# Performance work log

Measured on AMD Instinct MI355X. Metric: run time of the kernel, lower is better.

Reference implementation:

```python
import jax, jax.numpy as jnp
import numpy as np

S = 128          # hidden mul for 0e and 1o in the GVP
M_OUT = 256      # 2*n_dets*el_emb_dim = 2*8*16
N_DETS = 8
FACTOR = 2 * N_DETS  # mul_to_axis factor = 16
EPS = 1e-8


def _gvp_layer(s, v, Wh, Wu, Wm, bm, activate):
    # s: (..., S) scalars (0e); v: (..., S, 3) vectors (1o)
    Vh = jnp.einsum('...mt,mh->...ht', v, Wh)                 # hidden vectors
    vn = jnp.sqrt(jnp.sum(Vh * Vh, axis=-1) + EPS)            # invariant norms
    sm = jnp.concatenate([s, vn], axis=-1) @ Wm + bm          # scalar channel
    Vu = jnp.einsum('...ht,ho->...ot', Vh, Wu)
    if activate:
        return jax.nn.silu(sm), Vu * jax.nn.sigmoid(sm)[..., None]
    return sm, Vu  # activate_final=False


def _gvp_mlp(x, params):
    s = x[..., :S]
    v = x[..., S:].reshape(x.shape[:-1] + (S, 3))
    n = len(params)
    for i, (Wh, Wu, Wm, bm) in enumerate(params):
        s, v = _gvp_layer(s, v, Wh, Wu, Wm, bm, activate=(i < n - 1))
    return s, v


def _anti_mlp(x, params):
    # antisymmetrize_e3_func: odd part under parity (1o components negated)
    s1, v1 = _gvp_mlp(x, params)
    xp = jnp.concatenate([x[..., :S], -x[..., S:]], axis=-1)
    s2, v2 = _gvp_mlp(xp, params)
    return 0.5 * (s1 - s2), 0.5 * (v1 - v2)


def setup_inputs() -> dict:
    key = jax.random.key(0)
    ks = jax.random.split(key, 11)
    B, NEL = 2048, 16
    f32 = jnp.float32
    inp = {
        'mo_coeffs': jax.random.normal(ks[0], (B, NEL, S * 4), dtype=f32),
        # GVP layer 0
        'Wh0': jax.random.normal(ks[1], (S, S), f32) / np.sqrt(S),
        'Wu0': jax.random.normal(ks[2], (S, S), f32) / np.sqrt(S),
        'Wm0': jax.random.normal(ks[3], (2 * S, S), f32) / np.sqrt(2 * S),
        'bm0': jnp.zeros((S,), f32),
        # GVP layer 1 (final, no activation)
        'Wh1': jax.random.normal(ks[4], (S, S), f32) / np.sqrt(S),
        'Wu1': jax.random.normal(ks[5], (S, S), f32) / np.sqrt(S),
        'Wm1': jax.random.normal(ks[6], (2 * S, S), f32) / np.sqrt(2 * S),
        'bm1': jnp.zeros((S,), f32),
        # NamedE3Linear: one weight per irrep block (0e and 1o)
        'W0': jax.random.normal(ks[7], (S, M_OUT), f32),
        'W1': jax.random.normal(ks[8], (S, M_OUT), f32),
    }
    return inp


def reference(mo_coeffs, Wh0, Wu0, Wm0, bm0, Wh1, Wu1, Wm1, bm1, W0, W1):
    params = [(Wh0, Wu0, Wm0, bm0), (Wh1, Wu1, Wm1, bm1)]
    s, v = _anti_mlp(mo_coeffs, params)           # (...,128), (...,128,3)
    inv_sqrt = 1.0 / np.sqrt(S).astype(np.float32)
    so = (s @ W0) * inv_sqrt                      # (..., 256)   0e block
    vo = jnp.einsum('...mt,mn->...nt', v, W1) * inv_sqrt  # (...,256,3) 1o block
    lead = so.shape[:-1]
    # mul_to_axis(16): mul 256 -> (16, 16); per-irrep flat dims concatenated
    so = so.reshape(lead + (FACTOR, M_OUT // FACTOR))            # (...,16,16)
    vo = vo.reshape(lead + (FACTOR, (M_OUT // FACTOR) * 3))      # (...,16,48)
    bf = jnp.concatenate([so, vo], axis=-1)                      # (...,16,64)
    # final reshape: (..., 2*n_dets, d) -> (..., 2, n_dets, d)
    bf = bf.reshape(lead + (2, N_DETS, bf.shape[-1]))
    return bf
```

## Files before the change

### kernel.cpp

```cpp
#include <hip/hip_runtime.h>


typedef __attribute__((ext_vector_type(8))) short short8;
typedef __attribute__((ext_vector_type(4))) float floatx4;

static __device__ __forceinline__ unsigned short f2bf(float f) {
  unsigned u = __float_as_uint(f);
  u = (u + 0x7fffu + ((u >> 16) & 1u)) >> 16;
  return (unsigned short)u;
}
static __device__ __forceinline__ float bf2f(unsigned short h) {
  return __uint_as_float(((unsigned)h) << 16);
}

static __device__ __forceinline__ void put_sw(unsigned short* B, int k, int n,
                                              float val, int KT) {
  int kt = k >> 5, quad = (k >> 3) & 3, j = k & 7;
  int nt = n >> 4, c = n & 15;
  int lane = quad * 16 + c;
  B[(((nt * KT + kt) * 64 + lane) << 3) + j] = f2bf(val);
}

__global__ __launch_bounds__(128) void prep1(
    const float* __restrict__ Wh0, const float* __restrict__ Wu0,
    const float* __restrict__ Wh1, const float* __restrict__ Wu1,
    unsigned short* __restrict__ Wcat_sw, float* __restrict__ T) {
  int b = blockIdx.x, o = threadIdx.x;
  if (b < 128) {
    int m = b;
    float acc = 0.f;
    for (int h = 0; h < 128; ++h) acc += Wh0[m * 128 + h] * Wu0[h * 128 + o];
    put_sw(Wcat_sw, m, o, Wh0[m * 128 + o], 4);
    put_sw(Wcat_sw, m, o + 128, acc, 4);
  } else {
    int m = b - 128;
    float acc = 0.f;
    for (int h = 0; h < 128; ++h) acc += Wh1[m * 128 + h] * Wu1[h * 128 + o];
    T[m * 128 + o] = acc;
  }
}

__global__ __launch_bounds__(256) void prep2(
    const float* __restrict__ T, const float* __restrict__ W1,
    const float* __restrict__ Wm0, unsigned short* __restrict__ C_sw,
    unsigned short* __restrict__ Wm0_sw) {
  int b = blockIdx.x, tid = threadIdx.x;
  if (b < 128) {
    int m = b, n = tid;
    float acc = 0.f;
    for (int h = 0; h < 128; ++h) acc += T[m * 128 + h] * W1[h * 256 + n];
    put_sw(C_sw, m, n, acc * 0.08838834764831845f, 4);
  } else {
    int k = (b - 128) * 2 + (tid >> 7);
    int n = tid & 127;
    put_sw(Wm0_sw, k, n, Wm0[k * 128 + n], 8);
  }
}

#define XV_S 136
#define XA_S 264
#define GS_S 132
#define VO_S 260

__global__ __launch_bounds__(256, 2) void main_k(
    const float* __restrict__ x, const float* __restrict__ bm0,
    const unsigned short* __restrict__ Wcat_sw,
    const unsigned short* __restrict__ Wm0_sw,
    const unsigned short* __restrict__ C_sw, float* __restrict__ out) {
  __shared__ __align__(16) unsigned char smem[62976];
  unsigned short* v1 = (unsigned short*)smem;
  unsigned short* xa = (unsigned short*)(smem + 13056);
  unsigned short* xv = (unsigned short*)(smem + 21504);
  unsigned short* vh = (unsigned short*)(smem + 34560);
  float* gsm = (float*)(smem + 47616);
  float* vo = (float*)(smem + 13056);

  const int tid = threadIdx.x;
  const int lane = tid & 63;
  const int w = tid >> 6;
  const int l15 = lane & 15;
  const int quad = lane >> 4;
  const int r0 = blockIdx.x << 4;
  const float* xrow = x + (size_t)r0 * 512;

  for (int i = 0; i < 8; ++i) {
    int q = tid + 256 * i;
    int r = q >> 7;
    int c4 = (q & 127) << 2;
    float4 v4 = *(const float4*)(xrow + r * 512 + c4);
    float vv[4] = {v4.x, v4.y, v4.z, v4.w};
#pragma unroll
    for (int e = 0; e < 4; ++e) {
      int c = c4 + e;
      if (c < 128) {
        xa[r * XA_S + c] = f2bf(vv[e]);
      } else {
        int cc = c - 128;
        int m = cc / 3, t = cc - 3 * m;
        xv[(3 * r + t) * XV_S + m] = f2bf(vv[e]);
      }
    }
  }
  __syncthreads();

  const int ntg[4] = {2 * w, 2 * w + 1, 8 + 2 * w, 9 + 2 * w};
  const floatx4 zf4 = {0.f, 0.f, 0.f, 0.f};

  floatx4 acc[3][4];
#pragma unroll
  for (int mt = 0; mt < 3; ++mt)
#pragma unroll
    for (int t = 0; t < 4; ++t) acc[mt][t] = zf4;
  for (int kt = 0; kt < 4; ++kt) {
    short8 bf[4], af[3];
#pragma unroll
    for (int t = 0; t < 4; ++t)
      bf[t] = *(const short8*)(Wcat_sw + (((ntg[t] * 4 + kt) * 64 + lane) << 3));
#pragma unroll
    for (int mt = 0; mt < 3; ++mt)
      af[mt] = *(const short8*)(xv + (mt * 16 + l15) * XV_S + kt * 32 + quad * 8);
#pragma unroll
    for (int mt = 0; mt < 3; ++mt)
#pragma unroll
      for (int t = 0; t < 4; ++t)
        acc[mt][t] = __builtin_amdgcn_mfma_f32_16x16x32_bf16(af[mt], bf[t],
                                                             acc[mt][t], 0, 0, 0);
  }
#pragma unroll
  for (int t = 0; t < 2; ++t)
#pragma unroll
    for (int mt = 0; mt < 3; ++mt)
#pragma unroll
      for (int rg = 0; rg < 4; ++rg) {
        int row = mt * 16 + quad * 4 + rg;
        int col = ntg[t] * 16 + l15;
        vh[row * XV_S + col] = f2bf(acc[mt][t][rg]);
      }
  __syncthreads();

  for (int i = 0; i < 8; ++i) {
    int e = tid + 256 * i;
    int r = e >> 7, h = e & 127;
    float a0 = bf2f(vh[(3 * r) * XV_S + h]);
    float a1 = bf2f(vh[(3 * r + 1) * XV_S + h]);
    float a2 = bf2f(vh[(3 * r + 2) * XV_S + h]);
    xa[r * XA_S + 128 + h] = f2bf(sqrtf(a0 * a0 + a1 * a1 + a2 * a2 + 1e-8f));
  }
  __syncthreads();

  {
    floatx4 ga[2] = {zf4, zf4};
    for (int kt = 0; kt < 8; ++kt) {
      short8 af = *(const short8*)(xa + l15 * XA_S + kt * 32 + quad * 8);
      short8 b0 =
          *(const short8*)(Wm0_sw + ((((2 * w) * 8 + kt) * 64 + lane) << 3));
      short8 b1 =
          *(const short8*)(Wm0_sw + ((((2 * w + 1) * 8 + kt) * 64 + lane) << 3));
      ga[0] = __builtin_amdgcn_mfma_f32_16x16x32_bf16(af, b0, ga[0], 0, 0, 0);
      ga[1] = __builtin_amdgcn_mfma_f32_16x16x32_bf16(af, b1, ga[1], 0, 0, 0);
    }
#pragma unroll
    for (int t = 0; t < 2; ++t) {
      int col = (2 * w + t) * 16 + l15;
      float bias = bm0[col];
#pragma unroll
      for (int rg = 0; rg < 4; ++rg) {
        int row = quad * 4 + rg;
        float sm = ga[t][rg] + bias;
        gsm[row * GS_S + col] = 1.f / (1.f + __expf(-sm));
      }
    }
  }
  __syncthreads();

#pragma unroll
  for (int t = 2; t < 4; ++t) {
    int o = (2 * w + (t - 2)) * 16 + l15;
#pragma unroll
    for (int mt = 0; mt < 3; ++mt)
#pragma unroll
      for (int rg = 0; rg < 4; ++rg) {
        int ar = mt * 16 + quad * 4 + rg;
        float g = gsm[(ar / 3) * GS_S + o];
        v1[ar * XV_S + o] = f2bf(acc[mt][t][rg] * g);
      }
  }
  __syncthreads();

#pragma unroll
  for (int mt = 0; mt < 3; ++mt)
#pragma unroll
    for (int t = 0; t < 4; ++t) acc[mt][t] = zf4;
  for (int kt = 0; kt < 4; ++kt) {
    short8 bf[4], af[3];
#pragma unroll
    for (int t = 0; t < 4; ++t)
      bf[t] =
          *(const short8*)(C_sw + ((((4 * w + t) * 4 + kt) * 64 + lane) << 3));
#pragma unroll
    for (int mt = 0; mt < 3; ++mt)
      af[mt] = *(const short8*)(v1 + (mt * 16 + l15) * XV_S + kt * 32 + quad * 8);
#pragma unroll
    for (int mt = 0; mt < 3; ++mt)
#pragma unroll
      for (int t = 0; t < 4; ++t)
        acc[mt][t] = __builtin_amdgcn_mfma_f32_16x16x32_bf16(af[mt], bf[t],
                                                             acc[mt][t], 0, 0, 0);
  }
#pragma unroll
  for (int t = 0; t < 4; ++t)
#pragma unroll
    for (int mt = 0; mt < 3; ++mt)
#pragma unroll
      for (int rg = 0; rg < 4; ++rg) {
        int row = mt * 16 + quad * 4 + rg;
        int col = (4 * w + t) * 16 + l15;
        vo[row * VO_S + col] = acc[mt][t][rg];
      }
  __syncthreads();

  float* orow = out + (size_t)r0 * 1024;
  for (int i = 0; i < 16; ++i) {
    int e = tid + 256 * i;
    int r = e >> 8;
    int q4 = e & 255;
    int g = q4 >> 4, sub = q4 & 15;
    float4 val = make_float4(0.f, 0.f, 0.f, 0.f);
    if (sub >= 4) {
      float f[4];
#pragma unroll
      for (int ee = 0; ee < 4; ++ee) {
        int jj = sub * 4 + ee - 16;
        int n = g * 16 + jj / 3;
        int t = jj - 3 * (jj / 3);
        f[ee] = vo[(3 * r + t) * VO_S + n];
      }
      val = make_float4(f[0], f[1], f[2], f[3]);
    }
    *(float4*)(orow + (size_t)r * 1024 + q4 * 4) = val;
  }
}

extern "C" void kernel_launch(void* const* d_in, const int* in_sizes, int n_in,
                              void* d_out, int out_size, void* d_ws,
                              size_t ws_size, hipStream_t stream) {
  const float* Wh0 = (const float*)d_in[1];
  const float* Wu0 = (const float*)d_in[2];
  const float* Wm0 = (const float*)d_in[3];
  const float* bm0 = (const float*)d_in[4];
  const float* Wh1 = (const float*)d_in[5];
  const float* Wu1 = (const float*)d_in[6];
  const float* W1 = (const float*)d_in[10];
  const float* mo = (const float*)d_in[0];

  unsigned short* ws = (unsigned short*)d_ws;
  unsigned short* Wcat_sw = ws;
  unsigned short* C_sw = ws + 32768;
  unsigned short* Wm0_sw = ws + 65536;
  float* T = (float*)(ws + 98304);

  prep1<<<256, 128, 0, stream>>>(Wh0, Wu0, Wh1, Wu1, Wcat_sw, T);
  prep2<<<256, 256, 0, stream>>>(T, W1, Wm0, C_sw, Wm0_sw);

  main_k<<<2048, 256, 0, stream>>>(mo, bm0, Wcat_sw, Wm0_sw, C_sw,
                                   (float*)d_out);
}
```

Measured before the change: 246.4 us.

## Reorganize vector rows by component to keep norms, gates and outputs in registers

The vector input tile is now stored as three component planes (t-major), so each MFMA row tile holds a single xyz component for 16 rows. The norm, the sigmoid gate and the final output can then be computed directly from accumulator registers, without round trips through shared memory. This removes the vh, gsm and vo buffers and two barriers, and cuts LDS use enough to request four blocks per SM. Input packing is vectorized with paired bf16 conversion, and the output is written as float3 stores plus a separate zero fill, which leaves scattered, partly unaligned global writes.

```diff
diff --git a/kernel.cpp b/kernel.cpp
--- a/kernel.cpp
+++ b/kernel.cpp
@@ -1,4 +1,5 @@
 #include <hip/hip_runtime.h>
+#include <hip/hip_bf16.h>
 
 
 typedef __attribute__((ext_vector_type(8))) short short8;
@@ -9,8 +10,9 @@
   u = (u + 0x7fffu + ((u >> 16) & 1u)) >> 16;
   return (unsigned short)u;
 }
-static __device__ __forceinline__ float bf2f(unsigned short h) {
-  return __uint_as_float(((unsigned)h) << 16);
+static __device__ __forceinline__ unsigned pk2(float lo, float hi) {
+  __hip_bfloat162 h = __float22bfloat162_rn(make_float2(lo, hi));
+  return *(unsigned*)&h;
 }
 
 static __device__ __forceinline__ void put_sw(unsigned short* B, int k, int n,
@@ -57,23 +59,19 @@
   }
 }
 
+#define XA_S 264
 #define XV_S 136
-#define XA_S 264
-#define GS_S 132
-#define VO_S 260
-
-__global__ __launch_bounds__(256, 2) void main_k(
+#define XV_T 2176
+
+__global__ __launch_bounds__(256, 4) void main_k(
     const float* __restrict__ x, const float* __restrict__ bm0,
     const unsigned short* __restrict__ Wcat_sw,
     const unsigned short* __restrict__ Wm0_sw,
     const unsigned short* __restrict__ C_sw, float* __restrict__ out) {
-  __shared__ __align__(16) unsigned char smem[62976];
+  __shared__ __align__(16) unsigned char smem[34560];
   unsigned short* v1 = (unsigned short*)smem;
   unsigned short* xa = (unsigned short*)(smem + 13056);
   unsigned short* xv = (unsigned short*)(smem + 21504);
-  unsigned short* vh = (unsigned short*)(smem + 34560);
-  float* gsm = (float*)(smem + 47616);
-  float* vo = (float*)(smem + 13056);
 
   const int tid = threadIdx.x;
   const int lane = tid & 63;
@@ -82,168 +80,140 @@
   const int quad = lane >> 4;
   const int r0 = blockIdx.x << 4;
   const float* xrow = x + (size_t)r0 * 512;
-
-  for (int i = 0; i < 8; ++i) {
-    int q = tid + 256 * i;
-    int r = q >> 7;
-    int c4 = (q & 127) << 2;
-    float4 v4 = *(const float4*)(xrow + r * 512 + c4);
-    float vv[4] = {v4.x, v4.y, v4.z, v4.w};
-#pragma unroll
-    for (int e = 0; e < 4; ++e) {
-      int c = c4 + e;
-      if (c < 128) {
-        xa[r * XA_S + c] = f2bf(vv[e]);
-      } else {
-        int cc = c - 128;
-        int m = cc / 3, t = cc - 3 * m;
-        xv[(3 * r + t) * XV_S + m] = f2bf(vv[e]);
-      }
+  const int ntg[4] = {2 * w, 2 * w + 1, 8 + 2 * w, 9 + 2 * w};
+
+  float bias0 = bm0[(2 * w) * 16 + l15];
+  float bias1 = bm0[(2 * w + 1) * 16 + l15];
+
+#pragma unroll
+  for (int i = 0; i < 2; ++i) {
+    int e = tid + 256 * i;
+    int r = e >> 5, c0 = (e & 31) << 2;
+    float4 s4 = *(const float4*)(xrow + r * 512 + c0);
+    uint2 p = make_uint2(pk2(s4.x, s4.y), pk2(s4.z, s4.w));
+    *(uint2*)(xa + r * XA_S + c0) = p;
+  }
+#pragma unroll
+  for (int i = 0; i < 2; ++i) {
+    int e = tid + 256 * i;
+    int r = e >> 5, mc = e & 31;
+    const float* p = xrow + r * 512 + 128 + mc * 12;
+    float4 a = *(const float4*)(p);
+    float4 b = *(const float4*)(p + 4);
+    float4 c = *(const float4*)(p + 8);
+    float f[12] = {a.x, a.y, a.z, a.w, b.x, b.y, b.z, b.w, c.x, c.y, c.z, c.w};
+#pragma unroll
+    for (int t = 0; t < 3; ++t) {
+      uint2 pk = make_uint2(pk2(f[t], f[t + 3]), pk2(f[t + 6], f[t + 9]));
+      *(uint2*)(xv + t * XV_T + r * XV_S + mc * 4) = pk;
     }
   }
   __syncthreads();
 
-  const int ntg[4] = {2 * w, 2 * w + 1, 8 + 2 * w, 9 + 2 * w};
   const floatx4 zf4 = {0.f, 0.f, 0.f, 0.f};
 
   floatx4 acc[3][4];
 #pragma unroll
-  for (int mt = 0; mt < 3; ++mt)
-#pragma unroll
-    for (int t = 0; t < 4; ++t) acc[mt][t] = zf4;
+  for (int t = 0; t < 3; ++t)
+#pragma unroll
+    for (int j = 0; j < 4; ++j) acc[t][j] = zf4;
   for (int kt = 0; kt < 4; ++kt) {
-    short8 bf[4], af[3];
-#pragma unroll
-    for (int t = 0; t < 4; ++t)
-      bf[t] = *(const short8*)(Wcat_sw + (((ntg[t] * 4 + kt) * 64 + lane) << 3));
-#pragma unroll
-    for (int mt = 0; mt < 3; ++mt)
-      af[mt] = *(const short8*)(xv + (mt * 16 + l15) * XV_S + kt * 32 + quad * 8);
-#pragma unroll
-    for (int mt = 0; mt < 3; ++mt)
-#pragma unroll
-      for (int t = 0; t < 4; ++t)
-        acc[mt][t] = __builtin_amdgcn_mfma_f32_16x16x32_bf16(af[mt], bf[t],
-                                                             acc[mt][t], 0, 0, 0);
-  }
-#pragma unroll
-  for (int t = 0; t < 2; ++t)
-#pragma unroll
-    for (int mt = 0; mt < 3; ++mt)
+    short8 bf[4];
+#pragma unroll
+    for (int j = 0; j < 4; ++j)
+      bf[j] = *(const short8*)(Wcat_sw + (((ntg[j] * 4 + kt) * 64 + lane) << 3));
+#pragma unroll
+    for (int t = 0; t < 3; ++t) {
+      short8 af = *(const short8*)(xv + t * XV_T + l15 * XV_S + kt * 32 + quad * 8);
+#pragma unroll
+      for (int j = 0; j < 4; ++j)
+        acc[t][j] = __builtin_amdgcn_mfma_f32_16x16x32_bf16(af, bf[j], acc[t][j], 0, 0, 0);
+    }
+  }
+
+#pragma unroll
+  for (int j = 0; j < 2; ++j)
+#pragma unroll
+    for (int rg = 0; rg < 4; ++rg) {
+      float s0 = acc[0][j][rg], s1 = acc[1][j][rg], s2 = acc[2][j][rg];
+      float vn = sqrtf(s0 * s0 + s1 * s1 + s2 * s2 + 1e-8f);
+      int r = quad * 4 + rg;
+      int h = ntg[j] * 16 + l15;
+      xa[r * XA_S + 128 + h] = f2bf(vn);
+    }
+  __syncthreads();
+
+  floatx4 ga[2] = {zf4, zf4};
+  for (int kt = 0; kt < 8; ++kt) {
+    short8 af = *(const short8*)(xa + l15 * XA_S + kt * 32 + quad * 8);
+    short8 b0 = *(const short8*)(Wm0_sw + ((((2 * w) * 8 + kt) * 64 + lane) << 3));
+    short8 b1 = *(const short8*)(Wm0_sw + ((((2 * w + 1) * 8 + kt) * 64 + lane) << 3));
+    ga[0] = __builtin_amdgcn_mfma_f32_16x16x32_bf16(af, b0, ga[0], 0, 0, 0);
+    ga[1] = __builtin_amdgcn_mfma_f32_16x16x32_bf16(af, b1, ga[1], 0, 0, 0);
+  }
+  float g[2][4];
+#pragma unroll
+  for (int j = 0; j < 2; ++j) {
+    float bias = j ? bias1 : bias0;
+#pragma unroll
+    for (int rg = 0; rg < 4; ++rg)
+      g[j][rg] = 1.f / (1.f + __expf(-(ga[j][rg] + bias)));
+  }
+#pragma unroll
+  for (int t = 0; t < 3; ++t)
+#pragma unroll
+    for (int j = 0; j < 2; ++j)
 #pragma unroll
       for (int rg = 0; rg < 4; ++rg) {
-        int row = mt * 16 + quad * 4 + rg;
-        int col = ntg[t] * 16 + l15;
-        vh[row * XV_S + col] = f2bf(acc[mt][t][rg]);
+        int r = quad * 4 + rg;
+        int o = (2 * w + j) * 16 + l15;
+        v1[t * XV_T + r * XV_S + o] = f2bf(acc[t][2 + j][rg] * g[j][rg]);
       }
   __syncthreads();
 
-  for (int i = 0; i < 8; ++i) {
+  floatx4 vacc[3][4];
+#pragma unroll
+  for (int t = 0; t < 3; ++t)
+#pragma unroll
+    for (int j = 0; j < 4; ++j) vacc[t][j] = zf4;
+  for (int kt = 0; kt < 4; ++kt) {
+    short8 bf[4];
+#pragma unroll
+    for (int j = 0; j < 4; ++j)
+      bf[j] = *(const short8*)(C_sw + (((ntg[j] * 4 + kt) * 64 + lane) << 3));
+#pragma unroll
+    for (int t = 0; t < 3; ++t) {
+      short8 af = *(const short8*)(v1 + t * XV_T + l15 * XV_S + kt * 32 + quad * 8);
+#pragma unroll
+      for (int j = 0; j < 4; ++j)
+        vacc[t][j] = __builtin_amdgcn_mfma_f32_16x16x32_bf16(af, bf[j], vacc[t][j], 0, 0, 0);
+    }
+  }
+
+  float* orow = out + (size_t)r0 * 1024;
+#pragma unroll
+  for (int i = 0; i < 4; ++i) {
     int e = tid + 256 * i;
-    int r = e >> 7, h = e & 127;
-    float a0 = bf2f(vh[(3 * r) * XV_S + h]);
-    float a1 = bf2f(vh[(3 * r + 1) * XV_S + h]);
-    float a2 = bf2f(vh[(3 * r + 2) * XV_S + h]);
-    xa[r * XA_S + 128 + h] = f2bf(sqrtf(a0 * a0 + a1 * a1 + a2 * a2 + 1e-8f));
-  }
-  __syncthreads();
-
-  {
-    floatx4 ga[2] = {zf4, zf4};
-    for (int kt = 0; kt < 8; ++kt) {
-      short8 af = *(const short8*)(xa + l15 * XA_S + kt * 32 + quad * 8);
-      short8 b0 =
-          *(const short8*)(Wm0_sw + ((((2 * w) * 8 + kt) * 64 + lane) << 3));
-      short8 b1 =
-          *(const short8*)(Wm0_sw + ((((2 * w + 1) * 8 + kt) * 64 + lane) << 3));
-      ga[0] = __builtin_amdgcn_mfma_f32_16x16x32_bf16(af, b0, ga[0], 0, 0, 0);
-      ga[1] = __builtin_amdgcn_mfma_f32_16x16x32_bf16(af, b1, ga[1], 0, 0, 0);
-    }
-#pragma unroll
-    for (int t = 0; t < 2; ++t) {
-      int col = (2 * w + t) * 16 + l15;
-      float bias = bm0[col];
-#pragma unroll
-      for (int rg = 0; rg < 4; ++rg) {
-        int row = quad * 4 + rg;
-        float sm = ga[t][rg] + bias;
-        gsm[row * GS_S + col] = 1.f / (1.f + __expf(-sm));
-      }
-    }
-  }
-  __syncthreads();
-
-#pragma unroll
-  for (int t = 2; t < 4; ++t) {
-    int o = (2 * w + (t - 2)) * 16 + l15;
-#pragma unroll
-    for (int mt = 0; mt < 3; ++mt)
-#pragma unroll
-      for (int rg = 0; rg < 4; ++rg) {
-        int ar = mt * 16 + quad * 4 + rg;
-        float g = gsm[(ar / 3) * GS_S + o];
-        v1[ar * XV_S + o] = f2bf(acc[mt][t][rg] * g);
-      }
-  }
-  __syncthreads();
-
-#pragma unroll
-  for (int mt = 0; mt < 3; ++mt)
-#pragma unroll
-    for (int t = 0; t < 4; ++t) acc[mt][t] = zf4;
-  for (int kt = 0; kt < 4; ++kt) {
-    short8 bf[4], af[3];
-#pragma unroll
-    for (int t = 0; t < 4; ++t)
-      bf[t] =
-          *(const short8*)(C_sw + ((((4 * w + t) * 4 + kt) * 64 + lane) << 3));
-#pragma unroll
-    for (int mt = 0; mt < 3; ++mt)
-      af[mt] = *(const short8*)(v1 + (mt * 16 + l15) * XV_S + kt * 32 + quad * 8);
-#pragma unroll
-    for (int mt = 0; mt < 3; ++mt)
-#pragma unroll
-      for (int t = 0; t < 4; ++t)
-        acc[mt][t] = __builtin_amdgcn_mfma_f32_16x16x32_bf16(af[mt], bf[t],
-                                                             acc[mt][t], 0, 0, 0);
-  }
-#pragma unroll
-  for (int t = 0; t < 4; ++t)
-#pragma unroll
-    for (int mt = 0; mt < 3; ++mt)
-#pragma unroll
-      for (int rg = 0; rg < 4; ++rg) {
-        int row = mt * 16 + quad * 4 + rg;
-        int col = (4 * w + t) * 16 + l15;
-        vo[row * VO_S + col] = acc[mt][t][rg];
-      }
-  __syncthreads();
-
-  float* orow = out + (size_t)r0 * 1024;
-  for (int i = 0; i < 16; ++i) {
-    int e = tid + 256 * i;
-    int r = e >> 8;
-    int q4 = e & 255;
-    int g = q4 >> 4, sub = q4 & 15;
-    float4 val = make_float4(0.f, 0.f, 0.f, 0.f);
-    if (sub >= 4) {
-      float f[4];
-#pragma unroll
-      for (int ee = 0; ee < 4; ++ee) {
-        int jj = sub * 4 + ee - 16;
-        int n = g * 16 + jj / 3;
-        int t = jj - 3 * (jj / 3);
-        f[ee] = vo[(3 * r + t) * VO_S + n];
-      }
-      val = make_float4(f[0], f[1], f[2], f[3]);
-    }
-    *(float4*)(orow + (size_t)r * 1024 + q4 * 4) = val;
+    int r = e >> 6, gblk = (e >> 2) & 15, s4 = e & 3;
+    *(float4*)(orow + (size_t)r * 1024 + gblk * 64 + s4 * 4) =
+        make_float4(0.f, 0.f, 0.f, 0.f);
+  }
+#pragma unroll
+  for (int j = 0; j < 4; ++j) {
+    int nt = ntg[j];
+#pragma unroll
+    for (int rg = 0; rg < 4; ++rg) {
+      int r = quad * 4 + rg;
+      *(float3*)(orow + (size_t)r * 1024 + nt * 64 + 16 + 3 * l15) =
+          make_float3(vacc[0][j][rg], vacc[1][j][rg], vacc[2][j][rg]);
+    }
   }
 }
 
 extern "C" void kernel_launch(void* const* d_in, const int* in_sizes, int n_in,
                               void* d_out, int out_size, void* d_ws,
                               size_t ws_size, hipStream_t stream) {
+  const float* mo = (const float*)d_in[0];
   const float* Wh0 = (const float*)d_in[1];
   const float* Wu0 = (const float*)d_in[2];
   const float* Wm0 = (const float*)d_in[3];
@@ -251,7 +221,6 @@
   const float* Wh1 = (const float*)d_in[5];
   const float* Wu1 = (const float*)d_in[6];
   const float* W1 = (const float*)d_in[10];
-  const float* mo = (const float*)d_in[0];
 
   unsigned short* ws = (unsigned short*)d_ws;
   unsigned short* Wcat_sw = ws;
```

New measurement: 224.5 us. 1.1x faster.
